# Kernel tuning notes

Measured on AMD Instinct MI355X. Metric: run time of the kernel, lower is better.

## Reference

```python
import jax, jax.numpy as jnp
import numpy as np

EPS = 1e-5

def conv3(x, w, b):
    # 3x3 conv, stride 1, pad 1, NCHW/OIHW
    y = jax.lax.conv_general_dilated(x, w, (1, 1), ((1, 1), (1, 1)),
                                     dimension_numbers=('NCHW', 'OIHW', 'NCHW'))
    return y + b[None, :, None, None]

def positional_norm(x):
    # per-pixel channel-wise norm; torch .var() is unbiased (ddof=1)
    mean = jnp.mean(x, axis=1, keepdims=True)
    var = jnp.var(x, axis=1, keepdims=True, ddof=1)
    return (x - mean) / jnp.sqrt(var + EPS)

def bilinear_gather(x, py, px):
    # x: [B,C,H,W]; py/px: [B,K,H,W] absolute sample coords -> [B,C,K,H,W]
    B, C, H, W = x.shape
    K = py.shape[1]
    xf = x.reshape(B, C, H * W)
    y0 = jnp.floor(py).astype(jnp.int32)
    x0 = jnp.floor(px).astype(jnp.int32)
    wy = py - y0.astype(x.dtype)
    wx = px - x0.astype(x.dtype)

    def corner(yi, xi):
        valid = ((yi >= 0) & (yi < H) & (xi >= 0) & (xi < W)).astype(x.dtype)
        idx = (jnp.clip(yi, 0, H - 1) * W + jnp.clip(xi, 0, W - 1)).reshape(B, 1, K * H * W)
        v = jnp.take_along_axis(xf, idx, axis=2).reshape(B, C, K, H, W)
        return v * valid[:, None]

    out = ((1 - wy) * (1 - wx))[:, None] * corner(y0, x0)
    out = out + ((1 - wy) * wx)[:, None] * corner(y0, x0 + 1)
    out = out + (wy * (1 - wx))[:, None] * corner(y0 + 1, x0)
    out = out + (wy * wx)[:, None] * corner(y0 + 1, x0 + 1)
    return out

def dcn_v2(feat, cond, w_off, b_off, w_dcn, b_dcn):
    # DCNv2Pack: conv_offset(cond) -> (o1, o2, mask); modulated deformable 3x3 conv on feat
    B, C, H, W = feat.shape
    om = conv3(cond, w_off, b_off)                      # [B, 27, H, W]
    off = om[:, :18].reshape(B, 9, 2, H, W)             # (dy, dx) per kernel tap
    mask = jax.nn.sigmoid(om[:, 18:])                   # [B, 9, H, W]
    dy, dx = off[:, :, 0], off[:, :, 1]
    ki = jnp.repeat(jnp.arange(-1.0, 2.0, dtype=feat.dtype), 3)   # tap row offsets
    kj = jnp.tile(jnp.arange(-1.0, 2.0, dtype=feat.dtype), 3)     # tap col offsets
    hh = jnp.arange(H, dtype=feat.dtype)
    ww = jnp.arange(W, dtype=feat.dtype)
    py = dy + hh[None, None, :, None] + ki[None, :, None, None]
    px = dx + ww[None, None, None, :] + kj[None, :, None, None]
    sampled = bilinear_gather(feat, py, px)             # [B,C,9,H,W]
    wk = w_dcn.reshape(w_dcn.shape[0], C, 9)
    out = jnp.einsum('bkhw,bckhw,ock->bohw', mask, sampled, wk)
    return out + b_dcn[None, :, None, None]

def spade_forward(x, ref, w1, b1, w2, b2, w_off, b_off, w_dcn, b_dcn, w_g, b_g, w_be, b_be):
    normalized = positional_norm(x)
    h = jax.nn.relu(conv3(jnp.concatenate((normalized, ref), axis=1), w1, b1))
    cond = jax.nn.relu(conv3(h, w2, b2))
    ref_refine = dcn_v2(ref, cond, w_off, b_off, w_dcn, b_dcn)
    gamma = conv3(ref_refine, w_g, b_g)
    beta = conv3(ref_refine, w_be, b_be)
    return normalized * (1 + gamma) + beta

def setup_inputs() -> dict:
    key = jax.random.key(0)
    ks = jax.random.split(key, 16)
    B, NC, SC, H, W = 2, 64, 64, 96, 96
    mid = (NC + SC) // 8  # 16
    s = 0.05
    inp = {
        'x': jax.random.normal(ks[0], (B, NC, H, W), jnp.float32),
        'ref': jax.random.normal(ks[1], (B, SC, H, W), jnp.float32),
        'w1': jax.random.normal(ks[2], (mid, NC + SC, 3, 3), jnp.float32) * s,
        'b1': jax.random.normal(ks[3], (mid,), jnp.float32) * s,
        'w2': jax.random.normal(ks[4], (SC, mid, 3, 3), jnp.float32) * s,
        'b2': jax.random.normal(ks[5], (SC,), jnp.float32) * s,
        'w_off': jax.random.normal(ks[6], (27, SC, 3, 3), jnp.float32) * 0.01,
        'b_off': jax.random.normal(ks[7], (27,), jnp.float32) * 0.01,
        'w_dcn': jax.random.normal(ks[8], (SC, SC, 3, 3), jnp.float32) * s,
        'b_dcn': jax.random.normal(ks[9], (SC,), jnp.float32) * s,
        'w_g': jax.random.normal(ks[10], (NC, SC, 3, 3), jnp.float32) * s,
        'b_g': jax.random.normal(ks[11], (NC,), jnp.float32) * s,
        'w_be': jax.random.normal(ks[12], (NC, SC, 3, 3), jnp.float32) * s,
        'b_be': jax.random.normal(ks[13], (NC,), jnp.float32) * s,
    }
    return inp

def reference(x, ref, w1, b1, w2, b2, w_off, b_off, w_dcn, b_dcn, w_g, b_g, w_be, b_be):
    return spade_forward(x, ref, w1, b1, w2, b2, w_off, b_off, w_dcn, b_dcn, w_g, b_g, w_be, b_be)
```

## Files before the change

### kernel.cpp

```cpp
#include <hip/hip_runtime.h>
#include <math.h>

namespace {

typedef __attribute__((ext_vector_type(8))) short          bf16x8;
typedef __attribute__((ext_vector_type(8))) unsigned short u16x8;
typedef __attribute__((ext_vector_type(8))) _Float16       f16x8;
typedef __attribute__((ext_vector_type(4))) float          f32x4;

constexpr int B_  = 2;
constexpr int H_  = 96;
constexpr int W_  = 96;
constexpr int HW_ = H_ * W_;
constexpr int NC_ = 64;
constexpr int SC_ = 64;

__device__ inline unsigned short f2bf(float f) {
    union { float f; unsigned u; } v; v.f = f;
    unsigned r = v.u + 0x7FFFu + ((v.u >> 16) & 1u);
    return (unsigned short)(r >> 16);
}
__device__ inline unsigned short f2hbits(float f) {
    union { _Float16 h; unsigned short u; } s; s.h = (_Float16)f; return s.u;
}
__device__ inline _Float16 hfrombits(unsigned short u) {
    union { _Float16 h; unsigned short u; } s; s.u = u; return s.h;
}
__device__ inline bf16x8 ld_frag(const unsigned short* p) {
    return *reinterpret_cast<const bf16x8*>(p);
}

__global__ __launch_bounds__(256)
void prologue(const float* __restrict__ x, const float* __restrict__ ref,
              const float* __restrict__ w1, const float* __restrict__ w2,
              const float* __restrict__ woff, const float* __restrict__ wg,
              const float* __restrict__ wbe, const float* __restrict__ wdcn,
              float* __restrict__ nrm, unsigned short* __restrict__ cc,
              unsigned short* __restrict__ ccH,
              unsigned short* __restrict__ wt1, unsigned short* __restrict__ wt2,
              unsigned short* __restrict__ wtoff, unsigned short* __restrict__ wtg,
              unsigned short* __restrict__ wtbe, unsigned short* __restrict__ wbdH) {
    __shared__ float red1[4][64];
    __shared__ float red2[4][64];
    __shared__ float rtile[64][65];

    int blk = blockIdx.x;
    int t   = threadIdx.x;

    if (blk < 288) {
        int b  = blk / 144;
        int p0 = (blk % 144) * 64;
        int px = t & 63;
        int cg = t >> 6;
        int p  = p0 + px;

        float v[16];
        float s1 = 0.f, s2 = 0.f;
        const float* xb = x + ((size_t)b * NC_ + cg * 16) * HW_ + p;
        #pragma unroll
        for (int j = 0; j < 16; ++j) {
            v[j] = xb[j * HW_];
            s1 += v[j];
            s2 = fmaf(v[j], v[j], s2);
        }
        red1[cg][px] = s1;
        red2[cg][px] = s2;

        const float* rb = ref + (size_t)b * SC_ * HW_ + p0 + px;
        #pragma unroll
        for (int it = 0; it < 16; ++it) {
            int ch = it * 4 + cg;
            rtile[ch][px] = rb[(size_t)ch * HW_];
        }
        __syncthreads();

        s1 = red1[0][px] + red1[1][px] + red1[2][px] + red1[3][px];
        s2 = red2[0][px] + red2[1][px] + red2[2][px] + red2[3][px];
        float mean = s1 * (1.f / 64.f);
        float var  = (s2 - 64.f * mean * mean) * (1.f / 63.f);
        float inv  = 1.f / sqrtf(var + 1e-5f);
        float* nb = nrm + ((size_t)b * NC_ + cg * 16) * HW_ + p;
        u16x8 pk[2];
        #pragma unroll
        for (int j = 0; j < 16; ++j) {
            float nv = (v[j] - mean) * inv;
            nb[j * HW_] = nv;
            pk[j >> 3][j & 7] = f2bf(nv);
        }
        size_t bp = (size_t)b * HW_ + p;
        *reinterpret_cast<u16x8*>(&cc[bp * 128 + cg * 16 + 0]) = pk[0];
        *reinterpret_cast<u16x8*>(&cc[bp * 128 + cg * 16 + 8]) = pk[1];

        {
            int wpx = t >> 2, q = t & 3;
            size_t bp2 = (size_t)b * HW_ + p0 + wpx;
            u16x8 o0, o1, h0, h1;
            #pragma unroll
            for (int j = 0; j < 8; ++j) {
                float v0 = rtile[q * 16 + j][wpx];
                float v1 = rtile[q * 16 + 8 + j][wpx];
                o0[j] = f2bf(v0);    o1[j] = f2bf(v1);
                h0[j] = f2hbits(v0); h1[j] = f2hbits(v1);
            }
            *reinterpret_cast<u16x8*>(&cc[bp2 * 128 + 64 + q * 16 + 0]) = o0;
            *reinterpret_cast<u16x8*>(&cc[bp2 * 128 + 64 + q * 16 + 8]) = o1;
            *reinterpret_cast<u16x8*>(&ccH[bp2 * 64 + q * 16 + 0]) = h0;
            *reinterpret_cast<u16x8*>(&ccH[bp2 * 64 + q * 16 + 8]) = h1;
        }
    } else {
        int idx = (blk - 288) * 256 + t;
        if (idx < 9 * 16 * 128) {
            int tap = idx / (16 * 128), oc = (idx / 128) % 16, ic = idx % 128;
            wt1[idx] = f2bf(w1[(oc * 128 + ic) * 9 + tap]);
        }
        if (idx < 9 * 64 * 32) {
            int tap = idx / (64 * 32), oc = (idx / 32) % 64, ic = idx % 32;
            wt2[idx] = (ic < 16) ? f2bf(w2[(oc * 16 + ic) * 9 + tap]) : (unsigned short)0;
        }
        if (idx < 9 * 32 * 64) {
            int tap = idx / (32 * 64), oc = (idx / 64) % 32, ic = idx % 64;
            wtoff[idx] = (oc < 27) ? f2bf(woff[(oc * 64 + ic) * 9 + tap]) : (unsigned short)0;
        }
        if (idx < 9 * 64 * 64) {
            int tap = idx / (64 * 64), oc = (idx / 64) % 64, ic = idx % 64;
            wtg[idx]  = f2bf(wg [(oc * 64 + ic) * 9 + tap]);
            wtbe[idx] = f2bf(wbe[(oc * 64 + ic) * 9 + tap]);
        }
        if (idx < 64 * 576) {
            int oc = idx / 576, r = idx - oc * 576;
            int tap = r >> 6, ic = r & 63;
            wbdH[idx] = f2hbits(wdcn[oc * 576 + ic * 9 + tap]);
        }
    }
}

template <int R, int ICS, int ICP, int COLP, int COUT_PAD, int COUT_REAL,
          bool DUAL, bool RELU, int OMODE>
__global__ __launch_bounds__(256)
void conv_bf(const unsigned short* __restrict__ in,
             const unsigned short* __restrict__ Wt,
             const unsigned short* __restrict__ Wt2,
             const float* __restrict__ bias, const float* __restrict__ bias2,
             const float* __restrict__ nrm, float* __restrict__ outF,
             unsigned short* __restrict__ outB) {
    constexpr int NOCT = COUT_PAD / 16;
    constexpr int WPO  = 4 / NOCT;
    constexpr int MTP  = R / WPO;
    constexpr int NACC = DUAL ? 2 : 1;
    constexpr int NKS  = ICP / 32;
    constexpr int NCH8 = ICP / 8;
    constexpr int TY   = 96 / R;
    constexpr int PR   = R + 2;

    __shared__ unsigned short patch[PR * 18 * COLP];

    int t   = threadIdx.x;
    int blk = blockIdx.x;
    int bx  = blk % 6;
    int by  = (blk / 6) % TY;
    int b   = blk / (6 * TY);
    int x0  = bx * 16, y0 = by * R;

    for (int e = t; e < PR * 18 * NCH8; e += 256) {
        int kc  = e % NCH8;
        int col = (e / NCH8) % 18;
        int row = e / (NCH8 * 18);
        int yy = y0 + row - 1, xx = x0 + col - 1;
        bf16x8 v = (bf16x8){0, 0, 0, 0, 0, 0, 0, 0};
        if (kc * 8 < ICS && (unsigned)yy < (unsigned)H_ && (unsigned)xx < (unsigned)W_) {
            v = ld_frag(&in[((size_t)b * HW_ + yy * W_ + xx) * ICS + kc * 8]);
        }
        *reinterpret_cast<bf16x8*>(&patch[(row * 18 + col) * COLP + kc * 8]) = v;
    }
    __syncthreads();

    int wave = t >> 6, lane = t & 63;
    int fr = lane & 15, fq = lane >> 4;
    int oct  = wave / WPO;
    int widx = wave - oct * WPO;
    int mt0  = widx * MTP;

    f32x4 acc[MTP][NACC];
    #pragma unroll
    for (int i = 0; i < MTP; ++i)
        #pragma unroll
        for (int a = 0; a < NACC; ++a)
            acc[i][a] = (f32x4){0.f, 0.f, 0.f, 0.f};

    constexpr int dyv[9] = {0,0,0,1,1,1,2,2,2};
    constexpr int dxv[9] = {0,1,2,0,1,2,0,1,2};

    #pragma unroll
    for (int tap = 0; tap < 9; ++tap) {
        int dy = dyv[tap], dx = dxv[tap];
        #pragma unroll
        for (int ks = 0; ks < NKS; ++ks) {
            const size_t wo = ((size_t)tap * COUT_PAD + oct * 16 + fr) * ICP + ks * 32 + fq * 8;
            bf16x8 wfA = ld_frag(&Wt[wo]);
            bf16x8 wfB;
            if (DUAL) wfB = ld_frag(&Wt2[wo]);
            #pragma unroll
            for (int i = 0; i < MTP; ++i) {
                bf16x8 pf = ld_frag(&patch[((mt0 + i + dy) * 18 + (fr + dx)) * COLP
                                           + ks * 32 + fq * 8]);
                acc[i][0] = __builtin_amdgcn_mfma_f32_16x16x32_bf16(wfA, pf, acc[i][0], 0, 0, 0);
                if (DUAL)
                    acc[i][1] = __builtin_amdgcn_mfma_f32_16x16x32_bf16(wfB, pf, acc[i][1], 0, 0, 0);
            }
        }
    }

    #pragma unroll
    for (int i = 0; i < MTP; ++i) {
        int py = mt0 + i;
        if (OMODE == 1) {
            size_t p = (size_t)b * HW_ + (size_t)(y0 + py) * W_ + x0 + fr;
            ushort4 sv;
            #pragma unroll
            for (int j = 0; j < 4; ++j) {
                float v = acc[i][0][j] + bias[oct * 16 + fq * 4 + j];
                if (RELU) v = fmaxf(v, 0.f);
                ((unsigned short*)&sv)[j] = f2bf(v);
            }
            *reinterpret_cast<ushort4*>(&outB[p * COUT_REAL + oct * 16 + fq * 4]) = sv;
        } else {
            #pragma unroll
            for (int j = 0; j < 4; ++j) {
                int oc = oct * 16 + fq * 4 + j;
                if (oc >= COUT_REAL) continue;
                size_t off = ((size_t)b * COUT_REAL + oc) * HW_
                           + (size_t)(y0 + py) * W_ + x0 + fr;
                float v = acc[i][0][j] + bias[oc];
                if (DUAL) {
                    float be = acc[i][1][j] + bias2[oc];
                    float nv = nrm[off];
                    outF[off] = fmaf(nv, 1.f + v, be);
                } else {
                    outF[off] = RELU ? fmaxf(v, 0.f) : v;
                }
            }
        }
    }
}

constexpr int SROW = 584;
constexpr int DT   = 32;
constexpr int HMO  = 0;
constexpr int CNO  = 8192;

__global__ __launch_bounds__(256)
void dcn_kernel(const unsigned short* __restrict__ ccH,
                const unsigned short* __restrict__ hmidT,
                const unsigned short* __restrict__ wt2,
                const float* __restrict__ b2,
                const unsigned short* __restrict__ wtoff,
                const float* __restrict__ b_off,
                const unsigned short* __restrict__ wbdH,
                const float* __restrict__ b_dcn,
                unsigned short* __restrict__ rrT) {
    __shared__ unsigned short uS[DT * SROW];
    __shared__ float  omL[DT][36];
    __shared__ ushort4 cwLh[DT * 9];
    __shared__ int4    ciL[DT * 9];

    int t = threadIdx.x;
    int bid = blockIdx.x;
    int swz = (bid & 7) * 72 + (bid >> 3);
    int b   = swz / (HW_ / DT);
    int p0  = (swz % (HW_ / DT)) * DT;
    int y   = p0 / W_, x0 = p0 - y * W_;

    int wave = t >> 6, lane = t & 63;
    int fr = lane & 15, fq = lane >> 4;

    for (int e = t; e < 5 * 50 * 4; e += 256) {
        int kc  = e & 3;
        int col = (e >> 2) % 50;
        int row = (e >> 2) / 50;
        int yy = y + row - 2, xx = x0 + col - 2;
        bf16x8 v = (bf16x8){0, 0, 0, 0, 0, 0, 0, 0};
        if (kc < 2 && (unsigned)yy < (unsigned)H_ && (unsigned)xx < (unsigned)W_) {
            v = ld_frag(&hmidT[((size_t)b * HW_ + yy * W_ + xx) * 16 + kc * 8]);
        }
        *reinterpret_cast<bf16x8*>(&uS[HMO + (row * 50 + col) * 32 + kc * 8]) = v;
    }
    __syncthreads();

    {
        constexpr int dyv[9] = {0,0,0,1,1,1,2,2,2};
        constexpr int dxv[9] = {0,1,2,0,1,2,0,1,2};
        int oct = wave;
        #pragma unroll
        for (int mt = 0; mt < 9; ++mt) {
            int mr = mt / 3, mc = mt - mr * 3;
            int c  = mc * 16 + fr;
            f32x4 acc = (f32x4){0.f, 0.f, 0.f, 0.f};
            #pragma unroll
            for (int tap = 0; tap < 9; ++tap) {
                bf16x8 wf = ld_frag(&wt2[((size_t)tap * 64 + oct * 16 + fr) * 32 + fq * 8]);
                bf16x8 pf = *reinterpret_cast<const bf16x8*>(
                    &uS[HMO + ((mr + dyv[tap]) * 50 + c + dxv[tap]) * 32 + fq * 8]);
                acc = __builtin_amdgcn_mfma_f32_16x16x32_bf16(wf, pf, acc, 0, 0, 0);
            }
            if (c < 34) {
                int gy = y - 1 + mr, gx = x0 - 1 + c;
                bool inimg = ((unsigned)gy < (unsigned)H_) && ((unsigned)gx < (unsigned)W_);
                ushort4 sv;
                #pragma unroll
                for (int j = 0; j < 4; ++j) {
                    int oc = oct * 16 + fq * 4 + j;
                    float v = inimg ? fmaxf(acc[j] + b2[oc], 0.f) : 0.f;
                    ((unsigned short*)&sv)[j] = f2bf(v);
                }
                *reinterpret_cast<ushort4*>(&uS[CNO + (mr * 34 + c) * 72 + oct * 16 + fq * 4]) = sv;
            }
        }
    }
    __syncthreads();

    {
        int oct = wave & 1, mt = wave >> 1;
        f32x4 acc = (f32x4){0.f, 0.f, 0.f, 0.f};
        constexpr int dyv[9] = {0,0,0,1,1,1,2,2,2};
        constexpr int dxv[9] = {0,1,2,0,1,2,0,1,2};
        #pragma unroll
        for (int tap = 0; tap < 9; ++tap) {
            int dy = dyv[tap], dx = dxv[tap];
            #pragma unroll
            for (int ks = 0; ks < 2; ++ks) {
                bf16x8 wf = ld_frag(&wtoff[((size_t)tap * 32 + oct * 16 + fr) * 64
                                           + ks * 32 + fq * 8]);
                bf16x8 pf = *reinterpret_cast<const bf16x8*>(
                    &uS[CNO + (dy * 34 + mt * 16 + fr + dx) * 72 + ks * 32 + fq * 8]);
                acc = __builtin_amdgcn_mfma_f32_16x16x32_bf16(wf, pf, acc, 0, 0, 0);
            }
        }
        int px = mt * 16 + fr;
        float4 o4;
        #pragma unroll
        for (int j = 0; j < 4; ++j) {
            int oc = oct * 16 + fq * 4 + j;
            ((float*)&o4)[j] = acc[j] + (oc < 27 ? b_off[oc] : 0.f);
        }
        *reinterpret_cast<float4*>(&omL[px][oct * 16 + fq * 4]) = o4;
    }
    __syncthreads();

    for (int e = t; e < DT * 9; e += 256) {
        int pp = e / 9, k = e - pp * 9;
        int p  = p0 + pp;
        int yq = p / W_, xq = p - yq * W_;
        float dy = omL[pp][2 * k];
        float dx = omL[pp][2 * k + 1];
        float mk = omL[pp][18 + k];
        mk = 1.f / (1.f + expf(-mk));

        float py = dy + (float)yq + (float)(k / 3 - 1);
        float px = dx + (float)xq + (float)(k % 3 - 1);
        float fy = floorf(py), fx = floorf(px);
        int   y0c = (int)fy,  x0c = (int)fx;
        float wy = py - fy,   wx = px - fx;

        ushort4 cwh;
        int   ci[4];
        #pragma unroll
        for (int i = 0; i < 4; ++i) {
            int yy = y0c + (i >> 1);
            int xx = x0c + (i & 1);
            bool valid = (yy >= 0) && (yy < H_) && (xx >= 0) && (xx < W_);
            int yc = yy < 0 ? 0 : (yy > H_ - 1 ? H_ - 1 : yy);
            int xc = xx < 0 ? 0 : (xx > W_ - 1 ? W_ - 1 : xx);
            ci[i] = yc * W_ + xc;
            float wyi = (i >> 1) ? wy : (1.f - wy);
            float wxi = (i & 1)  ? wx : (1.f - wx);
            ((unsigned short*)&cwh)[i] = f2hbits(valid ? mk * wyi * wxi : 0.f);
        }
        cwLh[e] = cwh;
        ciL[e] = make_int4(ci[0], ci[1], ci[2], ci[3]);
    }
    __syncthreads();

    {
        const unsigned short* ch = ccH + (size_t)b * HW_ * 64;
        int pp = t >> 3, cg8 = t & 7;
        #pragma unroll
        for (int k = 0; k < 9; ++k) {
            ushort4 cwh = cwLh[pp * 9 + k];
            int4    ci  = ciL[pp * 9 + k];
            f16x8 r0 = *reinterpret_cast<const f16x8*>(&ch[(size_t)ci.x * 64 + cg8 * 8]);
            f16x8 r1 = *reinterpret_cast<const f16x8*>(&ch[(size_t)ci.y * 64 + cg8 * 8]);
            f16x8 r2 = *reinterpret_cast<const f16x8*>(&ch[(size_t)ci.z * 64 + cg8 * 8]);
            f16x8 r3 = *reinterpret_cast<const f16x8*>(&ch[(size_t)ci.w * 64 + cg8 * 8]);
            _Float16 h0 = hfrombits(cwh.x);
            _Float16 h1 = hfrombits(cwh.y);
            _Float16 h2 = hfrombits(cwh.z);
            _Float16 h3 = hfrombits(cwh.w);
            f16x8 s = r0 * h0;
            s += r1 * h1;
            s += r2 * h2;
            s += r3 * h3;
            *reinterpret_cast<f16x8*>(&uS[pp * SROW + k * 64 + cg8 * 8]) = s;
        }
    }
    __syncthreads();

    f32x4 acc0 = (f32x4){0.f, 0.f, 0.f, 0.f};
    f32x4 acc1 = (f32x4){0.f, 0.f, 0.f, 0.f};
    for (int ks = 0; ks < 18; ++ks) {
        f16x8 wf  = *reinterpret_cast<const f16x8*>(
            &wbdH[(size_t)(wave * 16 + fr) * 576 + ks * 32 + fq * 8]);
        f16x8 pf0 = *reinterpret_cast<const f16x8*>(
            &uS[(size_t)fr * SROW + ks * 32 + fq * 8]);
        f16x8 pf1 = *reinterpret_cast<const f16x8*>(
            &uS[(size_t)(16 + fr) * SROW + ks * 32 + fq * 8]);
        acc0 = __builtin_amdgcn_mfma_f32_16x16x32_f16(wf, pf0, acc0, 0, 0, 0);
        acc1 = __builtin_amdgcn_mfma_f32_16x16x32_f16(wf, pf1, acc1, 0, 0, 0);
    }

    {
        size_t p = (size_t)b * HW_ + p0 + fr;
        ushort4 sv0, sv1;
        #pragma unroll
        for (int j = 0; j < 4; ++j) {
            float bo = b_dcn[wave * 16 + fq * 4 + j];
            ((unsigned short*)&sv0)[j] = f2bf(acc0[j] + bo);
            ((unsigned short*)&sv1)[j] = f2bf(acc1[j] + bo);
        }
        *reinterpret_cast<ushort4*>(&rrT[p * 64 + wave * 16 + fq * 4]) = sv0;
        *reinterpret_cast<ushort4*>(&rrT[(p + 16) * 64 + wave * 16 + fq * 4]) = sv1;
    }
}

}

extern "C" void kernel_launch(void* const* d_in, const int* in_sizes, int n_in,
                              void* d_out, int out_size, void* d_ws, size_t ws_size,
                              hipStream_t stream) {
    (void)in_sizes; (void)n_in; (void)out_size; (void)ws_size;

    const float* x     = (const float*)d_in[0];
    const float* ref   = (const float*)d_in[1];
    const float* w1    = (const float*)d_in[2];
    const float* b1    = (const float*)d_in[3];
    const float* w2    = (const float*)d_in[4];
    const float* b2    = (const float*)d_in[5];
    const float* w_off = (const float*)d_in[6];
    const float* b_off = (const float*)d_in[7];
    const float* w_dcn = (const float*)d_in[8];
    const float* b_dcn = (const float*)d_in[9];
    const float* w_g   = (const float*)d_in[10];
    const float* b_g   = (const float*)d_in[11];
    const float* w_be  = (const float*)d_in[12];
    const float* b_be  = (const float*)d_in[13];

    float* out = (float*)d_out;
    float* ws  = (float*)d_ws;

    float* nrm = ws;
    unsigned short* cc    = (unsigned short*)(nrm + 1179648);
    unsigned short* ccH   = cc    + 2359296;
    unsigned short* hmidT = ccH   + 1179648;
    unsigned short* rrT   = hmidT + 294912;
    unsigned short* wt1   = rrT   + 1179648;
    unsigned short* wt2   = wt1   + 18432;
    unsigned short* wtoff = wt2   + 18432;
    unsigned short* wtg   = wtoff + 18432;
    unsigned short* wtbe  = wtg   + 36864;
    unsigned short* wbdH  = wtbe  + 36864;

    prologue<<<432, 256, 0, stream>>>(x, ref, w1, w2, w_off, w_g, w_be, w_dcn,
                                      nrm, cc, ccH, wt1, wt2, wtoff, wtg, wtbe, wbdH);

    conv_bf<4, 128, 128, 136, 16, 16, false, true, 1>
        <<<288, 256, 0, stream>>>(cc, wt1, nullptr, b1, nullptr, nullptr, nullptr, hmidT);

    dcn_kernel<<<B_ * (HW_ / DT), 256, 0, stream>>>(ccH, hmidT, wt2, b2,
                                                    wtoff, b_off, wbdH, b_dcn, rrT);

    conv_bf<2, 64, 64, 72, 64, 64, true, false, 0>
        <<<576, 256, 0, stream>>>(rrT, wtg, wtbe, b_g, b_be, nrm, out, nullptr);
}
```

Before: 68.59 us.

## Split conv1 by input-channel chunks, move conv2 out of DCN kernel, shrink tiles

Conv1 (128 to 16 channels) is now split over four input-channel chunks. Each chunk writes fp32 partial sums, and a new conv2 kernel reduces them, adds bias and ReLU, and computes the 16 to 64 conv into a bf16 cond tensor. The DCN kernel no longer recomputes conv2 on a 5x50 halo and just loads the cond tile. The prologue and the final gamma/beta conv use smaller tiles, launching more blocks for better occupancy. In exchange the code adds an extra launch and extra global traffic for the partial sums and the cond tensor.

```diff
diff --git a/kernel.cpp b/kernel.cpp
--- a/kernel.cpp
+++ b/kernel.cpp
@@ -14,6 +14,7 @@
 constexpr int HW_ = H_ * W_;
 constexpr int NC_ = 64;
 constexpr int SC_ = 64;
+constexpr size_t HPCH = (size_t)B_ * HW_ * 16;
 
 __device__ inline unsigned short f2bf(float f) {
     union { float f; unsigned u; } v; v.f = f;
@@ -40,25 +41,25 @@
               unsigned short* __restrict__ wt1, unsigned short* __restrict__ wt2,
               unsigned short* __restrict__ wtoff, unsigned short* __restrict__ wtg,
               unsigned short* __restrict__ wtbe, unsigned short* __restrict__ wbdH) {
-    __shared__ float red1[4][64];
-    __shared__ float red2[4][64];
-    __shared__ float rtile[64][65];
+    __shared__ float red1[8][32];
+    __shared__ float red2[8][32];
+    __shared__ float rtile[64][33];
 
     int blk = blockIdx.x;
     int t   = threadIdx.x;
 
-    if (blk < 288) {
-        int b  = blk / 144;
-        int p0 = (blk % 144) * 64;
-        int px = t & 63;
-        int cg = t >> 6;
+    if (blk < 576) {
+        int b  = blk / 288;
+        int p0 = (blk % 288) * 32;
+        int px = t & 31;
+        int cg = t >> 5;
         int p  = p0 + px;
 
-        float v[16];
+        float v[8];
         float s1 = 0.f, s2 = 0.f;
-        const float* xb = x + ((size_t)b * NC_ + cg * 16) * HW_ + p;
-        #pragma unroll
-        for (int j = 0; j < 16; ++j) {
+        const float* xb = x + ((size_t)b * NC_ + cg * 8) * HW_ + p;
+        #pragma unroll
+        for (int j = 0; j < 8; ++j) {
             v[j] = xb[j * HW_];
             s1 += v[j];
             s2 = fmaf(v[j], v[j], s2);
@@ -66,49 +67,45 @@
         red1[cg][px] = s1;
         red2[cg][px] = s2;
 
-        const float* rb = ref + (size_t)b * SC_ * HW_ + p0 + px;
-        #pragma unroll
-        for (int it = 0; it < 16; ++it) {
-            int ch = it * 4 + cg;
-            rtile[ch][px] = rb[(size_t)ch * HW_];
-        }
+        const float* rb = ref + (size_t)b * SC_ * HW_ + p;
+        #pragma unroll
+        for (int j = 0; j < 8; ++j)
+            rtile[cg * 8 + j][px] = rb[(size_t)(cg * 8 + j) * HW_];
         __syncthreads();
 
-        s1 = red1[0][px] + red1[1][px] + red1[2][px] + red1[3][px];
-        s2 = red2[0][px] + red2[1][px] + red2[2][px] + red2[3][px];
+        s1 = 0.f; s2 = 0.f;
+        #pragma unroll
+        for (int k = 0; k < 8; ++k) { s1 += red1[k][px]; s2 += red2[k][px]; }
         float mean = s1 * (1.f / 64.f);
         float var  = (s2 - 64.f * mean * mean) * (1.f / 63.f);
         float inv  = 1.f / sqrtf(var + 1e-5f);
-        float* nb = nrm + ((size_t)b * NC_ + cg * 16) * HW_ + p;
-        u16x8 pk[2];
-        #pragma unroll
-        for (int j = 0; j < 16; ++j) {
+
+        float* nb = nrm + ((size_t)b * NC_ + cg * 8) * HW_ + p;
+        u16x8 pk;
+        #pragma unroll
+        for (int j = 0; j < 8; ++j) {
             float nv = (v[j] - mean) * inv;
             nb[j * HW_] = nv;
-            pk[j >> 3][j & 7] = f2bf(nv);
+            pk[j] = f2bf(nv);
         }
         size_t bp = (size_t)b * HW_ + p;
-        *reinterpret_cast<u16x8*>(&cc[bp * 128 + cg * 16 + 0]) = pk[0];
-        *reinterpret_cast<u16x8*>(&cc[bp * 128 + cg * 16 + 8]) = pk[1];
+        *reinterpret_cast<u16x8*>(&cc[bp * 128 + cg * 8]) = pk;
 
         {
-            int wpx = t >> 2, q = t & 3;
+            int wpx = t >> 3, q = t & 7;
             size_t bp2 = (size_t)b * HW_ + p0 + wpx;
-            u16x8 o0, o1, h0, h1;
+            u16x8 o, h;
             #pragma unroll
             for (int j = 0; j < 8; ++j) {
-                float v0 = rtile[q * 16 + j][wpx];
-                float v1 = rtile[q * 16 + 8 + j][wpx];
-                o0[j] = f2bf(v0);    o1[j] = f2bf(v1);
-                h0[j] = f2hbits(v0); h1[j] = f2hbits(v1);
+                float v0 = rtile[q * 8 + j][wpx];
+                o[j] = f2bf(v0);
+                h[j] = f2hbits(v0);
             }
-            *reinterpret_cast<u16x8*>(&cc[bp2 * 128 + 64 + q * 16 + 0]) = o0;
-            *reinterpret_cast<u16x8*>(&cc[bp2 * 128 + 64 + q * 16 + 8]) = o1;
-            *reinterpret_cast<u16x8*>(&ccH[bp2 * 64 + q * 16 + 0]) = h0;
-            *reinterpret_cast<u16x8*>(&ccH[bp2 * 64 + q * 16 + 8]) = h1;
+            *reinterpret_cast<u16x8*>(&cc[bp2 * 128 + 64 + q * 8]) = o;
+            *reinterpret_cast<u16x8*>(&ccH[bp2 * 64 + q * 8]) = h;
         }
     } else {
-        int idx = (blk - 288) * 256 + t;
+        int idx = (blk - 576) * 256 + t;
         if (idx < 9 * 16 * 128) {
             int tap = idx / (16 * 128), oc = (idx / 128) % 16, ic = idx % 128;
             wt1[idx] = f2bf(w1[(oc * 128 + ic) * 9 + tap]);
@@ -134,19 +131,122 @@
     }
 }
 
+__global__ __launch_bounds__(256)
+void conv1_part(const unsigned short* __restrict__ cc,
+                const unsigned short* __restrict__ wt1,
+                float* __restrict__ hpart) {
+    __shared__ unsigned short patch[6 * 18 * 40];
+
+    int t = threadIdx.x;
+    int blk = blockIdx.x;
+    int chunk = blk & 3;
+    int tile  = blk >> 2;
+    int bx = tile % 6, by = (tile / 6) % 24, b = tile / 144;
+    int x0 = bx * 16, y0 = by * 4;
+
+    for (int e = t; e < 6 * 18 * 4; e += 256) {
+        int kc  = e & 3;
+        int col = (e >> 2) % 18;
+        int row = (e >> 2) / 18;
+        int yy = y0 + row - 1, xx = x0 + col - 1;
+        bf16x8 v = (bf16x8){0, 0, 0, 0, 0, 0, 0, 0};
+        if ((unsigned)yy < (unsigned)H_ && (unsigned)xx < (unsigned)W_) {
+            v = ld_frag(&cc[((size_t)b * HW_ + yy * W_ + xx) * 128 + chunk * 32 + kc * 8]);
+        }
+        *reinterpret_cast<bf16x8*>(&patch[(row * 18 + col) * 40 + kc * 8]) = v;
+    }
+    __syncthreads();
+
+    int wave = t >> 6, lane = t & 63;
+    int fr = lane & 15, fq = lane >> 4;
+
+    f32x4 acc = (f32x4){0.f, 0.f, 0.f, 0.f};
+    constexpr int dyv[9] = {0,0,0,1,1,1,2,2,2};
+    constexpr int dxv[9] = {0,1,2,0,1,2,0,1,2};
+    #pragma unroll
+    for (int tap = 0; tap < 9; ++tap) {
+        bf16x8 wf = ld_frag(&wt1[((size_t)tap * 16 + fr) * 128 + chunk * 32 + fq * 8]);
+        bf16x8 pf = ld_frag(&patch[((wave + dyv[tap]) * 18 + (fr + dxv[tap])) * 40 + fq * 8]);
+        acc = __builtin_amdgcn_mfma_f32_16x16x32_bf16(wf, pf, acc, 0, 0, 0);
+    }
+
+    size_t p = (size_t)b * HW_ + (size_t)(y0 + wave) * W_ + x0 + fr;
+    *reinterpret_cast<f32x4*>(&hpart[(size_t)chunk * HPCH + p * 16 + fq * 4]) = acc;
+}
+
+__global__ __launch_bounds__(256)
+void conv2_k(const float* __restrict__ hpart, const float* __restrict__ b1,
+             const unsigned short* __restrict__ wt2, const float* __restrict__ b2,
+             unsigned short* __restrict__ condT) {
+    __shared__ unsigned short patch[3 * 18 * 40];
+
+    int t = threadIdx.x;
+    int blk = blockIdx.x;
+    int bx = blk % 6;
+    int y0 = (blk / 6) % 96;
+    int b  = blk / 576;
+    int x0 = bx * 16;
+
+    for (int e = t; e < 3 * 18 * 4; e += 256) {
+        int kc  = e & 3;
+        int col = (e >> 2) % 18;
+        int row = (e >> 2) / 18;
+        int yy = y0 + row - 1, xx = x0 + col - 1;
+        u16x8 sv = (u16x8){0, 0, 0, 0, 0, 0, 0, 0};
+        if (kc < 2 && (unsigned)yy < (unsigned)H_ && (unsigned)xx < (unsigned)W_) {
+            size_t off = ((size_t)b * HW_ + yy * W_ + xx) * 16 + kc * 8;
+            f32x4 lo = (f32x4){0.f, 0.f, 0.f, 0.f};
+            f32x4 hi = (f32x4){0.f, 0.f, 0.f, 0.f};
+            #pragma unroll
+            for (int c = 0; c < 4; ++c) {
+                lo += *reinterpret_cast<const f32x4*>(&hpart[c * HPCH + off]);
+                hi += *reinterpret_cast<const f32x4*>(&hpart[c * HPCH + off + 4]);
+            }
+            #pragma unroll
+            for (int j = 0; j < 4; ++j) {
+                sv[j]     = f2bf(fmaxf(lo[j] + b1[kc * 8 + j], 0.f));
+                sv[4 + j] = f2bf(fmaxf(hi[j] + b1[kc * 8 + 4 + j], 0.f));
+            }
+        }
+        *reinterpret_cast<u16x8*>(&patch[(row * 18 + col) * 40 + kc * 8]) = sv;
+    }
+    __syncthreads();
+
+    int wave = t >> 6, lane = t & 63;
+    int fr = lane & 15, fq = lane >> 4;
+    int oct = wave;
+
+    f32x4 acc = (f32x4){0.f, 0.f, 0.f, 0.f};
+    constexpr int dyv[9] = {0,0,0,1,1,1,2,2,2};
+    constexpr int dxv[9] = {0,1,2,0,1,2,0,1,2};
+    #pragma unroll
+    for (int tap = 0; tap < 9; ++tap) {
+        bf16x8 wf = ld_frag(&wt2[((size_t)tap * 64 + oct * 16 + fr) * 32 + fq * 8]);
+        bf16x8 pf = ld_frag(&patch[((dyv[tap]) * 18 + (fr + dxv[tap])) * 40 + fq * 8]);
+        acc = __builtin_amdgcn_mfma_f32_16x16x32_bf16(wf, pf, acc, 0, 0, 0);
+    }
+
+    size_t p = (size_t)b * HW_ + (size_t)y0 * W_ + x0 + fr;
+    ushort4 sv;
+    #pragma unroll
+    for (int j = 0; j < 4; ++j) {
+        float v = fmaxf(acc[j] + b2[oct * 16 + fq * 4 + j], 0.f);
+        ((unsigned short*)&sv)[j] = f2bf(v);
+    }
+    *reinterpret_cast<ushort4*>(&condT[p * 64 + oct * 16 + fq * 4]) = sv;
+}
+
 template <int R, int ICS, int ICP, int COLP, int COUT_PAD, int COUT_REAL,
-          bool DUAL, bool RELU, int OMODE>
+          bool DUAL, bool RELU>
 __global__ __launch_bounds__(256)
 void conv_bf(const unsigned short* __restrict__ in,
              const unsigned short* __restrict__ Wt,
              const unsigned short* __restrict__ Wt2,
              const float* __restrict__ bias, const float* __restrict__ bias2,
-             const float* __restrict__ nrm, float* __restrict__ outF,
-             unsigned short* __restrict__ outB) {
+             const float* __restrict__ nrm, float* __restrict__ outF) {
     constexpr int NOCT = COUT_PAD / 16;
     constexpr int WPO  = 4 / NOCT;
     constexpr int MTP  = R / WPO;
-    constexpr int NACC = DUAL ? 2 : 1;
     constexpr int NKS  = ICP / 32;
     constexpr int NCH8 = ICP / 8;
     constexpr int TY   = 96 / R;
@@ -180,12 +280,12 @@
     int widx = wave - oct * WPO;
     int mt0  = widx * MTP;
 
-    f32x4 acc[MTP][NACC];
+    f32x4 accA[MTP], accB[MTP];
     #pragma unroll
-    for (int i = 0; i < MTP; ++i)
-        #pragma unroll
-        for (int a = 0; a < NACC; ++a)
-            acc[i][a] = (f32x4){0.f, 0.f, 0.f, 0.f};
+    for (int i = 0; i < MTP; ++i) {
+        accA[i] = (f32x4){0.f, 0.f, 0.f, 0.f};
+        accB[i] = (f32x4){0.f, 0.f, 0.f, 0.f};
+    }
 
     constexpr int dyv[9] = {0,0,0,1,1,1,2,2,2};
     constexpr int dxv[9] = {0,1,2,0,1,2,0,1,2};
@@ -203,9 +303,9 @@
             for (int i = 0; i < MTP; ++i) {
                 bf16x8 pf = ld_frag(&patch[((mt0 + i + dy) * 18 + (fr + dx)) * COLP
                                            + ks * 32 + fq * 8]);
-                acc[i][0] = __builtin_amdgcn_mfma_f32_16x16x32_bf16(wfA, pf, acc[i][0], 0, 0, 0);
+                accA[i] = __builtin_amdgcn_mfma_f32_16x16x32_bf16(wfA, pf, accA[i], 0, 0, 0);
                 if (DUAL)
-                    acc[i][1] = __builtin_amdgcn_mfma_f32_16x16x32_bf16(wfB, pf, acc[i][1], 0, 0, 0);
+                    accB[i] = __builtin_amdgcn_mfma_f32_16x16x32_bf16(wfB, pf, accB[i], 0, 0, 0);
             }
         }
     }
@@ -213,31 +313,19 @@
     #pragma unroll
     for (int i = 0; i < MTP; ++i) {
         int py = mt0 + i;
-        if (OMODE == 1) {
-            size_t p = (size_t)b * HW_ + (size_t)(y0 + py) * W_ + x0 + fr;
-            ushort4 sv;
-            #pragma unroll
-            for (int j = 0; j < 4; ++j) {
-                float v = acc[i][0][j] + bias[oct * 16 + fq * 4 + j];
-                if (RELU) v = fmaxf(v, 0.f);
-                ((unsigned short*)&sv)[j] = f2bf(v);
-            }
-            *reinterpret_cast<ushort4*>(&outB[p * COUT_REAL + oct * 16 + fq * 4]) = sv;
-        } else {
-            #pragma unroll
-            for (int j = 0; j < 4; ++j) {
-                int oc = oct * 16 + fq * 4 + j;
-                if (oc >= COUT_REAL) continue;
-                size_t off = ((size_t)b * COUT_REAL + oc) * HW_
-                           + (size_t)(y0 + py) * W_ + x0 + fr;
-                float v = acc[i][0][j] + bias[oc];
-                if (DUAL) {
-                    float be = acc[i][1][j] + bias2[oc];
-                    float nv = nrm[off];
-                    outF[off] = fmaf(nv, 1.f + v, be);
-                } else {
-                    outF[off] = RELU ? fmaxf(v, 0.f) : v;
-                }
+        #pragma unroll
+        for (int j = 0; j < 4; ++j) {
+            int oc = oct * 16 + fq * 4 + j;
+            if (oc >= COUT_REAL) continue;
+            size_t off = ((size_t)b * COUT_REAL + oc) * HW_
+                       + (size_t)(y0 + py) * W_ + x0 + fr;
+            float v = accA[i][j] + bias[oc];
+            if (DUAL) {
+                float be = accB[i][j] + bias2[oc];
+                float nv = nrm[off];
+                outF[off] = fmaf(nv, 1.f + v, be);
+            } else {
+                outF[off] = RELU ? fmaxf(v, 0.f) : v;
             }
         }
     }
@@ -245,14 +333,10 @@
 
 constexpr int SROW = 584;
 constexpr int DT   = 32;
-constexpr int HMO  = 0;
-constexpr int CNO  = 8192;
 
 __global__ __launch_bounds__(256)
 void dcn_kernel(const unsigned short* __restrict__ ccH,
-                const unsigned short* __restrict__ hmidT,
-                const unsigned short* __restrict__ wt2,
-                const float* __restrict__ b2,
+                const unsigned short* __restrict__ condT,
                 const unsigned short* __restrict__ wtoff,
                 const float* __restrict__ b_off,
                 const unsigned short* __restrict__ wbdH,
@@ -270,53 +354,21 @@
     int p0  = (swz % (HW_ / DT)) * DT;
     int y   = p0 / W_, x0 = p0 - y * W_;
 
+    for (int e = t; e < 3 * 34 * 8; e += 256) {
+        int kc  = e & 7;
+        int col = (e >> 3) % 34;
+        int row = (e >> 3) / 34;
+        int yy = y + row - 1, xx = x0 + col - 1;
+        bf16x8 v = (bf16x8){0, 0, 0, 0, 0, 0, 0, 0};
+        if ((unsigned)yy < (unsigned)H_ && (unsigned)xx < (unsigned)W_) {
+            v = ld_frag(&condT[((size_t)b * HW_ + yy * W_ + xx) * 64 + kc * 8]);
+        }
+        *reinterpret_cast<bf16x8*>(&uS[(row * 34 + col) * 72 + kc * 8]) = v;
+    }
+    __syncthreads();
+
     int wave = t >> 6, lane = t & 63;
     int fr = lane & 15, fq = lane >> 4;
-
-    for (int e = t; e < 5 * 50 * 4; e += 256) {
-        int kc  = e & 3;
-        int col = (e >> 2) % 50;
-        int row = (e >> 2) / 50;
-        int yy = y + row - 2, xx = x0 + col - 2;
-        bf16x8 v = (bf16x8){0, 0, 0, 0, 0, 0, 0, 0};
-        if (kc < 2 && (unsigned)yy < (unsigned)H_ && (unsigned)xx < (unsigned)W_) {
-            v = ld_frag(&hmidT[((size_t)b * HW_ + yy * W_ + xx) * 16 + kc * 8]);
-        }
-        *reinterpret_cast<bf16x8*>(&uS[HMO + (row * 50 + col) * 32 + kc * 8]) = v;
-    }
-    __syncthreads();
-
-    {
-        constexpr int dyv[9] = {0,0,0,1,1,1,2,2,2};
-        constexpr int dxv[9] = {0,1,2,0,1,2,0,1,2};
-        int oct = wave;
-        #pragma unroll
-        for (int mt = 0; mt < 9; ++mt) {
-            int mr = mt / 3, mc = mt - mr * 3;
-            int c  = mc * 16 + fr;
-            f32x4 acc = (f32x4){0.f, 0.f, 0.f, 0.f};
-            #pragma unroll
-            for (int tap = 0; tap < 9; ++tap) {
-                bf16x8 wf = ld_frag(&wt2[((size_t)tap * 64 + oct * 16 + fr) * 32 + fq * 8]);
-                bf16x8 pf = *reinterpret_cast<const bf16x8*>(
-                    &uS[HMO + ((mr + dyv[tap]) * 50 + c + dxv[tap]) * 32 + fq * 8]);
-                acc = __builtin_amdgcn_mfma_f32_16x16x32_bf16(wf, pf, acc, 0, 0, 0);
-            }
-            if (c < 34) {
-                int gy = y - 1 + mr, gx = x0 - 1 + c;
-                bool inimg = ((unsigned)gy < (unsigned)H_) && ((unsigned)gx < (unsigned)W_);
-                ushort4 sv;
-                #pragma unroll
-                for (int j = 0; j < 4; ++j) {
-                    int oc = oct * 16 + fq * 4 + j;
-                    float v = inimg ? fmaxf(acc[j] + b2[oc], 0.f) : 0.f;
-                    ((unsigned short*)&sv)[j] = f2bf(v);
-                }
-                *reinterpret_cast<ushort4*>(&uS[CNO + (mr * 34 + c) * 72 + oct * 16 + fq * 4]) = sv;
-            }
-        }
-    }
-    __syncthreads();
 
     {
         int oct = wave & 1, mt = wave >> 1;
@@ -331,7 +383,7 @@
                 bf16x8 wf = ld_frag(&wtoff[((size_t)tap * 32 + oct * 16 + fr) * 64
                                            + ks * 32 + fq * 8]);
                 bf16x8 pf = *reinterpret_cast<const bf16x8*>(
-                    &uS[CNO + (dy * 34 + mt * 16 + fr + dx) * 72 + ks * 32 + fq * 8]);
+                    &uS[(dy * 34 + mt * 16 + fr + dx) * 72 + ks * 32 + fq * 8]);
                 acc = __builtin_amdgcn_mfma_f32_16x16x32_bf16(wf, pf, acc, 0, 0, 0);
             }
         }
@@ -456,11 +508,12 @@
     float* out = (float*)d_out;
     float* ws  = (float*)d_ws;
 
-    float* nrm = ws;
-    unsigned short* cc    = (unsigned short*)(nrm + 1179648);
+    float* nrm   = ws;
+    float* hpart = nrm + 1179648;
+    unsigned short* cc    = (unsigned short*)(hpart + 1179648);
     unsigned short* ccH   = cc    + 2359296;
-    unsigned short* hmidT = ccH   + 1179648;
-    unsigned short* rrT   = hmidT + 294912;
+    unsigned short* condT = ccH   + 1179648;
+    unsigned short* rrT   = condT + 1179648;
     unsigned short* wt1   = rrT   + 1179648;
     unsigned short* wt2   = wt1   + 18432;
     unsigned short* wtoff = wt2   + 18432;
@@ -468,15 +521,15 @@
     unsigned short* wtbe  = wtg   + 36864;
     unsigned short* wbdH  = wtbe  + 36864;
 
-    prologue<<<432, 256, 0, stream>>>(x, ref, w1, w2, w_off, w_g, w_be, w_dcn,
+    prologue<<<720, 256, 0, stream>>>(x, ref, w1, w2, w_off, w_g, w_be, w_dcn,
                                       nrm, cc, ccH, wt1, wt2, wtoff, wtg, wtbe, wbdH);
 
-    conv_bf<4, 128, 128, 136, 16, 16, false, true, 1>
-        <<<288, 256, 0, stream>>>(cc, wt1, nullptr, b1, nullptr, nullptr, nullptr, hmidT);
-
-    dcn_kernel<<<B_ * (HW_ / DT), 256, 0, stream>>>(ccH, hmidT, wt2, b2,
-                                                    wtoff, b_off, wbdH, b_dcn, rrT);
-
-    conv_bf<2, 64, 64, 72, 64, 64, true, false, 0>
-        <<<576, 256, 0, stream>>>(rrT, wtg, wtbe, b_g, b_be, nrm, out, nullptr);
-}
+    conv1_part<<<1152, 256, 0, stream>>>(cc, wt1, hpart);
+
+    conv2_k<<<1152, 256, 0, stream>>>(hpart, b1, wt2, b2, condT);
+
+    dcn_kernel<<<576, 256, 0, stream>>>(ccH, condT, wtoff, b_off, wbdH, b_dcn, rrT);
+
+    conv_bf<1, 64, 64, 72, 64, 64, true, false>
+        <<<1152, 256, 0, stream>>>(rrT, wtg, wtbe, b_g, b_be, nrm, out);
+}
```

Measured after the change: 72.20 us. +5.3%, slower.
